# Kernel optimization log

Hardware: AMD Instinct MI355X
Metric: run time of the kernel (lower is better)

## Reference

```python
import jax, jax.numpy as jnp
import numpy as np

B, N, E, K = 8, 4096, 1, 3
F = [16, 32, 16]
MLP_HID, MLP_OUT = 64, 1


def graph_filter(x, S, h, b):
    # x: [B, Fin, N], S: [E, N, N], h: [Fout, E, K, Fin], b: [Fout, 1]
    Bx, Fin, Nx = x.shape
    Ex, Kx = h.shape[1], h.shape[2]
    cur = jnp.broadcast_to(x[:, None], (Bx, Ex, Fin, Nx))  # tap 0: z = x
    zs = [cur]
    for _ in range(Kx - 1):
        cur = jnp.einsum('enm,befm->befn', S, cur)  # diffuse one hop
        zs.append(cur)
    z = jnp.stack(zs, axis=2)  # [B, E, K, Fin, N]
    return jnp.einsum('gekf,bekfn->bgn', h, z) + b[None]  # [B, Fout, N]


def gnn_layer(x, S, h, b, n_out):
    # GraphFilter -> ReLU -> NoPool (select first n_out nodes)
    return jax.nn.relu(graph_filter(x, S, h, b))[:, :, :n_out]


def setup_inputs() -> dict:
    key = jax.random.key(0)
    ks = jax.random.split(key, 16)
    sN = np.float32(1.0 / np.sqrt(N))
    x = jax.random.normal(ks[0], (B, F[0], N), dtype=jnp.float32)
    S_clique = jax.random.normal(ks[1], (E, N, N), dtype=jnp.float32) * sN
    S_line = jax.random.normal(ks[2], (E, N, N), dtype=jnp.float32) * sN

    def w(k, fo, fi):
        s = np.float32(1.0 / np.sqrt(fi * K))
        return jax.random.normal(k, (fo, E, K, fi), dtype=jnp.float32) * s

    Wc1, bc1 = w(ks[3], F[1], F[0]), jnp.zeros((F[1], 1), jnp.float32)
    Wc2, bc2 = w(ks[4], F[2], F[1]), jnp.zeros((F[2], 1), jnp.float32)
    Wl1, bl1 = w(ks[5], F[1], F[0]), jnp.zeros((F[1], 1), jnp.float32)
    Wl2, bl2 = w(ks[6], F[2], F[1]), jnp.zeros((F[2], 1), jnp.float32)
    d_in = N * F[-1]
    Wm1 = jax.random.normal(ks[7], (MLP_HID, d_in), dtype=jnp.float32) * np.float32(1.0 / np.sqrt(d_in))
    bm1 = jnp.zeros((MLP_HID,), jnp.float32)
    Wm2 = jax.random.normal(ks[8], (MLP_OUT, MLP_HID), dtype=jnp.float32) * np.float32(1.0 / np.sqrt(MLP_HID))
    bm2 = jnp.zeros((MLP_OUT,), jnp.float32)
    return {'x': x, 'S_clique': S_clique, 'S_line': S_line,
            'Wc1': Wc1, 'bc1': bc1, 'Wc2': Wc2, 'bc2': bc2,
            'Wl1': Wl1, 'bl1': bl1, 'Wl2': Wl2, 'bl2': bl2,
            'Wm1': Wm1, 'bm1': bm1, 'Wm2': Wm2, 'bm2': bm2}


def reference(x, S_clique, S_line, Wc1, bc1, Wc2, bc2, Wl1, bl1, Wl2, bl2, Wm1, bm1, Wm2, bm2):
    # clique-expansion branch (L=2 layers)
    y = gnn_layer(x, S_clique, Wc1, bc1, N)
    y = gnn_layer(y, S_clique, Wc2, bc2, N)
    # line-expansion branch (L=2 layers)
    y = gnn_layer(y, S_line, Wl1, bl1, N)
    y = gnn_layer(y, S_line, Wl2, bl2, N)
    yFlat = y.reshape(y.shape[0], -1)  # [B, F[-1]*N] (row-major matches torch)
    h = jax.nn.relu(yFlat @ Wm1.T + bm1)
    return h @ Wm2.T + bm2  # [B, 1]
```

## Files before the change

kernel.cpp:

```cpp
#include <hip/hip_runtime.h>


#define NN 4096
#define BB 8

typedef unsigned short u16;
typedef unsigned int   u32;

typedef __attribute__((ext_vector_type(8))) short bf16x8;
typedef __attribute__((ext_vector_type(4))) float f32x4;

__device__ __forceinline__ u16 f2bf(float f) {
    union { float f; u32 i; } c; c.f = f;
    u32 i = c.i;
    u32 r = (i + 0x7FFFu + ((i >> 16) & 1u)) >> 16;
    return (u16)r;
}
__device__ __forceinline__ float bf2f(u16 u) {
    union { u32 i; float f; } c; c.i = ((u32)u) << 16; return c.f;
}
__device__ __forceinline__ u32 pack2bf(float lo, float hi) {
    return (u32)f2bf(lo) | ((u32)f2bf(hi) << 16);
}

__device__ __forceinline__ void gload_lds16(const u16* g, u16* l) {
    __builtin_amdgcn_global_load_lds(
        (__attribute__((address_space(1))) void*)g,
        (__attribute__((address_space(3))) void*)l, 16, 0, 0);
}

__global__ __launch_bounds__(256) void cvt_x(const float* __restrict__ in,
                                             u16* __restrict__ out)
{
    const int i = (blockIdx.x * 256 + threadIdx.x) * 8;
    float4 a = *(const float4*)(in + i);
    float4 b = *(const float4*)(in + i + 4);
    uint4 o;
    o.x = pack2bf(a.x, a.y); o.y = pack2bf(a.z, a.w);
    o.z = pack2bf(b.x, b.y); o.w = pack2bf(b.z, b.w);
    *(uint4*)(out + i) = o;
}

template <int ITERS>
__global__ __launch_bounds__(256) void diffuse_cvtB(const u16* __restrict__ Z,
                                                    const float* __restrict__ Sf,
                                                    u16* __restrict__ Part,
                                                    u16* __restrict__ Sb)
{
    __shared__ u16 As[2 * 128 * 64];
    __shared__ u16 Bs[2 * 64 * 64];

    const int bx    = blockIdx.x;
    const int ntile = ((bx & 7) << 3) | (bx >> 3);
    const int nBase = ntile * 64;
    const int mBase = blockIdx.y * 128;
    const int tid   = threadIdx.x;
    const int lane  = tid & 63;
    const int wv    = tid >> 6;
    const int quad  = lane >> 4;
    const int l16   = lane & 15;

    const int kStart = (int)blockIdx.z * (ITERS * 64);

    const int rl   = lane >> 3;
    const int gsl  = lane & 7;
    const int gsrc = gsl ^ rl;

    f32x4 acc[2][4];
#pragma unroll
    for (int i = 0; i < 2; ++i)
#pragma unroll
        for (int j = 0; j < 4; ++j) acc[i][j] = (f32x4){0.f, 0.f, 0.f, 0.f};

    auto stageA = [&](int buf, int k0) {
#pragma unroll
        for (int j = 0; j < 4; ++j) {
            const int rb = (wv * 4 + j) * 8;
            gload_lds16(Z + (size_t)(mBase + rb + rl) * NN + k0 + gsrc * 8,
                        &As[buf * 8192 + rb * 64]);
        }
    };

    float4 fB[2][2];
    auto loadB = [&](int k0) {
#pragma unroll
        for (int j = 0; j < 2; ++j) {
            const int row = nBase + (wv * 2 + j) * 8 + rl;
            const float* p = Sf + (size_t)row * NN + k0 + gsrc * 8;
            fB[j][0] = *(const float4*)p;
            fB[j][1] = *(const float4*)(p + 4);
        }
    };
    auto writeB = [&](int buf, int k0) {
#pragma unroll
        for (int j = 0; j < 2; ++j) {
            const int rloc = (wv * 2 + j) * 8 + rl;
            bf16x8 v;
            v[0] = (short)f2bf(fB[j][0].x); v[1] = (short)f2bf(fB[j][0].y);
            v[2] = (short)f2bf(fB[j][0].z); v[3] = (short)f2bf(fB[j][0].w);
            v[4] = (short)f2bf(fB[j][1].x); v[5] = (short)f2bf(fB[j][1].y);
            v[6] = (short)f2bf(fB[j][1].z); v[7] = (short)f2bf(fB[j][1].w);
            *(bf16x8*)&Bs[buf * 4096 + rloc * 64 + gsl * 8] = v;
            *(bf16x8*)&Sb[(size_t)(nBase + rloc) * NN + k0 + gsrc * 8] = v;
        }
    };

    auto compute = [&](int buf) {
#pragma unroll
        for (int s = 0; s < 2; ++s) {
            const int g = s * 4 + quad;
            bf16x8 af[2], bf[4];
#pragma unroll
            for (int mi = 0; mi < 2; ++mi) {
                const int r = wv * 32 + mi * 16 + l16;
                af[mi] = *(const bf16x8*)&As[buf * 8192 + r * 64 + ((g ^ (r & 7)) << 3)];
            }
#pragma unroll
            for (int ni = 0; ni < 4; ++ni) {
                const int r = ni * 16 + l16;
                bf[ni] = *(const bf16x8*)&Bs[buf * 4096 + r * 64 + ((g ^ (r & 7)) << 3)];
            }
#pragma unroll
            for (int mi = 0; mi < 2; ++mi)
#pragma unroll
                for (int ni = 0; ni < 4; ++ni)
                    acc[mi][ni] = __builtin_amdgcn_mfma_f32_16x16x32_bf16(
                        af[mi], bf[ni], acc[mi][ni], 0, 0, 0);
        }
    };

    loadB(kStart);
    stageA(0, kStart);
    writeB(0, kStart);
    __syncthreads();

#pragma unroll
    for (int i = 0; i < ITERS; ++i) {
        const int cur = i & 1;
        if (i + 1 < ITERS) {
            stageA(cur ^ 1, kStart + (i + 1) * 64);
            loadB(kStart + (i + 1) * 64);
        }
        compute(cur);
        if (i + 1 < ITERS) writeB(cur ^ 1, kStart + (i + 1) * 64);
        __syncthreads();
    }

    u16* tb = &As[wv * 2304];
#pragma unroll
    for (int mi = 0; mi < 2; ++mi)
#pragma unroll
        for (int ni = 0; ni < 4; ++ni)
#pragma unroll
            for (int i = 0; i < 4; ++i)
                tb[(mi * 16 + quad * 4 + i) * 72 + ni * 16 + l16] =
                    f2bf(acc[mi][ni][i]);

    const size_t plane = (size_t)gridDim.y * 128 * NN;
    u16* pp = Part + (size_t)blockIdx.z * plane;
    const int row0g = mBase + wv * 32;
#pragma unroll
    for (int j = 0; j < 4; ++j) {
        const int r = (lane >> 3) + j * 8;
        const int c = (lane & 7) * 8;
        bf16x8 v = *(const bf16x8*)&tb[r * 72 + c];
        *(bf16x8*)&pp[(size_t)(row0g + r) * NN + nBase + c] = v;
    }
}

template <int ITERS>
__global__ __launch_bounds__(256) void diffuse(const u16* __restrict__ Z,
                                               const u16* __restrict__ S,
                                               u16* __restrict__ Part)
{
    __shared__ u16 As[3 * 128 * 64];
    __shared__ u16 Bs[3 * 64 * 64];

    const int bx    = blockIdx.x;
    const int ntile = ((bx & 7) << 3) | (bx >> 3);
    const int nBase = ntile * 64;
    const int mBase = blockIdx.y * 128;
    const int tid   = threadIdx.x;
    const int lane  = tid & 63;
    const int wv    = tid >> 6;
    const int quad  = lane >> 4;
    const int l16   = lane & 15;

    const int kStart = (int)blockIdx.z * (ITERS * 64);

    const int rl   = lane >> 3;
    const int gsl  = lane & 7;
    const int gsrc = gsl ^ rl;

    f32x4 acc[2][4];
#pragma unroll
    for (int i = 0; i < 2; ++i)
#pragma unroll
        for (int j = 0; j < 4; ++j) acc[i][j] = (f32x4){0.f, 0.f, 0.f, 0.f};

    auto stage = [&](int buf, int k0) {
#pragma unroll
        for (int j = 0; j < 4; ++j) {
            const int rb = (wv * 4 + j) * 8;
            gload_lds16(Z + (size_t)(mBase + rb + rl) * NN + k0 + gsrc * 8,
                        &As[buf * 8192 + rb * 64]);
        }
#pragma unroll
        for (int j = 0; j < 2; ++j) {
            const int rb = (wv * 2 + j) * 8;
            gload_lds16(S + (size_t)(nBase + rb + rl) * NN + k0 + gsrc * 8,
                        &Bs[buf * 4096 + rb * 64]);
        }
    };

    auto compute = [&](int buf) {
#pragma unroll
        for (int s = 0; s < 2; ++s) {
            const int g = s * 4 + quad;
            bf16x8 af[2], bf[4];
#pragma unroll
            for (int mi = 0; mi < 2; ++mi) {
                const int r = wv * 32 + mi * 16 + l16;
                af[mi] = *(const bf16x8*)&As[buf * 8192 + r * 64 + ((g ^ (r & 7)) << 3)];
            }
#pragma unroll
            for (int ni = 0; ni < 4; ++ni) {
                const int r = ni * 16 + l16;
                bf[ni] = *(const bf16x8*)&Bs[buf * 4096 + r * 64 + ((g ^ (r & 7)) << 3)];
            }
#pragma unroll
            for (int mi = 0; mi < 2; ++mi)
#pragma unroll
                for (int ni = 0; ni < 4; ++ni)
                    acc[mi][ni] = __builtin_amdgcn_mfma_f32_16x16x32_bf16(
                        af[mi], bf[ni], acc[mi][ni], 0, 0, 0);
        }
    };

    stage(0, kStart);
    stage(1, kStart + 64);

#pragma unroll
    for (int i = 0; i < ITERS; ++i) {
        if (i + 2 < ITERS) stage((i + 2) % 3, kStart + (i + 2) * 64);
        if (i < ITERS - 2)
            asm volatile("s_waitcnt vmcnt(12)" ::: "memory");
        else if (i == ITERS - 2)
            asm volatile("s_waitcnt vmcnt(6)" ::: "memory");
        else
            asm volatile("s_waitcnt vmcnt(0)" ::: "memory");
        __builtin_amdgcn_s_barrier();
        compute(i % 3);
        if (i + 1 < ITERS) __builtin_amdgcn_s_barrier();
    }

    asm volatile("s_waitcnt lgkmcnt(0)" ::: "memory");
    __builtin_amdgcn_s_barrier();

    u16* tb = &As[wv * 2304];
#pragma unroll
    for (int mi = 0; mi < 2; ++mi)
#pragma unroll
        for (int ni = 0; ni < 4; ++ni)
#pragma unroll
            for (int i = 0; i < 4; ++i)
                tb[(mi * 16 + quad * 4 + i) * 72 + ni * 16 + l16] =
                    f2bf(acc[mi][ni][i]);

    const size_t plane = (size_t)gridDim.y * 128 * NN;
    u16* pp = Part + (size_t)blockIdx.z * plane;
    const int row0g = mBase + wv * 32;
#pragma unroll
    for (int j = 0; j < 4; ++j) {
        const int r = (lane >> 3) + j * 8;
        const int c = (lane & 7) * 8;
        bf16x8 v = *(const bf16x8*)&tb[r * 72 + c];
        *(bf16x8*)&pp[(size_t)(row0g + r) * NN + nBase + c] = v;
    }
}

template <int KS>
__global__ __launch_bounds__(256) void reduce_part(const u16* __restrict__ part,
                                                   int planeElems,
                                                   u16* __restrict__ outb)
{
    const int base   = (blockIdx.x * 256 + threadIdx.x) * 8;
    const int stride = gridDim.x * 256 * 8;
    for (int i = base; i < planeElems; i += stride) {
        float s[8];
#pragma unroll
        for (int e = 0; e < 8; ++e) s[e] = 0.f;
#pragma unroll
        for (int p = 0; p < KS; ++p) {
            uint4 v = *(const uint4*)(part + (size_t)p * planeElems + i);
            const u32 w[4] = {v.x, v.y, v.z, v.w};
#pragma unroll
            for (int q = 0; q < 4; ++q) {
                union { u32 i; float f; } lo, hi;
                lo.i = w[q] << 16;
                hi.i = w[q] & 0xFFFF0000u;
                s[q * 2]     += lo.f;
                s[q * 2 + 1] += hi.f;
            }
        }
        uint4 o;
        o.x = (u32)f2bf(s[0]) | ((u32)f2bf(s[1]) << 16);
        o.y = (u32)f2bf(s[2]) | ((u32)f2bf(s[3]) << 16);
        o.z = (u32)f2bf(s[4]) | ((u32)f2bf(s[5]) << 16);
        o.w = (u32)f2bf(s[6]) | ((u32)f2bf(s[7]) << 16);
        *(uint4*)(outb + i) = o;
    }
}

template <int FIN, int FOUT, int KS>
__global__ __launch_bounds__(256) void combine_relu(
    const u16* __restrict__ z0, const u16* __restrict__ z1,
    const u16* __restrict__ part2, int planeElems,
    const float* __restrict__ W, const float* __restrict__ bias,
    u16* __restrict__ out)
{
    __shared__ float hs[FOUT * 3 * FIN];
    __shared__ float bs[FOUT];
    for (int i = threadIdx.x; i < FOUT * 3 * FIN; i += 256) hs[i] = W[i];
    if (threadIdx.x < FOUT) bs[threadIdx.x] = bias[threadIdx.x];
    __syncthreads();

    const int nb = NN / 256;
    const int b  = blockIdx.x / nb;
    const int n  = (blockIdx.x % nb) * 256 + threadIdx.x;

    float zv[3][FIN];
    const u16* zp0 = z0 + (size_t)b * FIN * NN + n;
    const u16* zp1 = z1 + (size_t)b * FIN * NN + n;
    const u16* zp2 = part2 + (size_t)b * FIN * NN + n;
#pragma unroll
    for (int f = 0; f < FIN; ++f) {
        zv[0][f] = bf2f(zp0[(size_t)f * NN]);
        zv[1][f] = bf2f(zp1[(size_t)f * NN]);
        float s = 0.f;
#pragma unroll
        for (int p = 0; p < KS; ++p)
            s += bf2f(zp2[(size_t)p * planeElems + (size_t)f * NN]);
        zv[2][f] = s;
    }

    u16* op = out + (size_t)b * FOUT * NN + n;
    for (int g = 0; g < FOUT; ++g) {
        float acc = bs[g];
#pragma unroll
        for (int k = 0; k < 3; ++k)
#pragma unroll
            for (int f = 0; f < FIN; ++f)
                acc = fmaf(hs[(g * 3 + k) * FIN + f], zv[k][f], acc);
        op[(size_t)g * NN] = f2bf(fmaxf(acc, 0.f));
    }
}

__global__ __launch_bounds__(256) void mlp1(const u16* __restrict__ y,
                                            const float* __restrict__ Wm1,
                                            float* __restrict__ h1p)
{
    const int j    = blockIdx.x;
    const int base = blockIdx.y * 8192;
    const int D    = 16 * NN;

    float acc[BB];
#pragma unroll
    for (int b = 0; b < BB; ++b) acc[b] = 0.f;

    const float* wrow = Wm1 + (size_t)j * D + base;
    for (int idx = threadIdx.x * 8; idx < 8192; idx += 256 * 8) {
        float4 w0 = *(const float4*)(wrow + idx);
        float4 w1 = *(const float4*)(wrow + idx + 4);
#pragma unroll
        for (int b = 0; b < BB; ++b) {
            uint4 yv = *(const uint4*)(y + (size_t)b * D + base + idx);
            union { u32 i; float f; } c[8];
            c[0].i = yv.x << 16; c[1].i = yv.x & 0xFFFF0000u;
            c[2].i = yv.y << 16; c[3].i = yv.y & 0xFFFF0000u;
            c[4].i = yv.z << 16; c[5].i = yv.z & 0xFFFF0000u;
            c[6].i = yv.w << 16; c[7].i = yv.w & 0xFFFF0000u;
            acc[b] = fmaf(w0.x, c[0].f, acc[b]);
            acc[b] = fmaf(w0.y, c[1].f, acc[b]);
            acc[b] = fmaf(w0.z, c[2].f, acc[b]);
            acc[b] = fmaf(w0.w, c[3].f, acc[b]);
            acc[b] = fmaf(w1.x, c[4].f, acc[b]);
            acc[b] = fmaf(w1.y, c[5].f, acc[b]);
            acc[b] = fmaf(w1.z, c[6].f, acc[b]);
            acc[b] = fmaf(w1.w, c[7].f, acc[b]);
        }
    }

    __shared__ float red[BB][4];
    const int lane = threadIdx.x & 63;
    const int w    = threadIdx.x >> 6;
#pragma unroll
    for (int b = 0; b < BB; ++b) {
        float v = acc[b];
        for (int off = 32; off > 0; off >>= 1) v += __shfl_down(v, off, 64);
        if (lane == 0) red[b][w] = v;
    }
    __syncthreads();
    if (threadIdx.x < BB) {
        const int b = threadIdx.x;
        h1p[blockIdx.y * (BB * 64) + b * 64 + j] =
            red[b][0] + red[b][1] + red[b][2] + red[b][3];
    }
}

__global__ void mlp2(const float* __restrict__ h1p,
                     const float* __restrict__ bm1,
                     const float* __restrict__ Wm2,
                     const float* __restrict__ bm2, float* __restrict__ out)
{
    const int lane = threadIdx.x;
    const float w    = Wm2[lane];
    const float b1   = bm1[lane];
    const float bias = bm2[0];
    for (int b = 0; b < BB; ++b) {
        float h = 0.f;
#pragma unroll
        for (int p = 0; p < 8; ++p) h += h1p[p * (BB * 64) + b * 64 + lane];
        float v = fmaxf(h + b1, 0.f) * w;
        for (int off = 32; off > 0; off >>= 1) v += __shfl_down(v, off, 64);
        if (lane == 0) out[b] = v + bias;
    }
}

extern "C" void kernel_launch(void* const* d_in, const int* in_sizes, int n_in,
                              void* d_out, int out_size, void* d_ws, size_t ws_size,
                              hipStream_t stream)
{
    const float* x   = (const float*)d_in[0];
    const float* Sc  = (const float*)d_in[1];
    const float* Sl  = (const float*)d_in[2];
    const float* Wc1 = (const float*)d_in[3];
    const float* bc1 = (const float*)d_in[4];
    const float* Wc2 = (const float*)d_in[5];
    const float* bc2 = (const float*)d_in[6];
    const float* Wl1 = (const float*)d_in[7];
    const float* bl1 = (const float*)d_in[8];
    const float* Wl2 = (const float*)d_in[9];
    const float* bl2 = (const float*)d_in[10];
    const float* Wm1 = (const float*)d_in[11];
    const float* bm1 = (const float*)d_in[12];
    const float* Wm2 = (const float*)d_in[13];
    const float* bm2 = (const float*)d_in[14];
    float* out = (float*)d_out;

    char* ws = (char*)d_ws;
    u16*   part = (u16*)(ws);
    u16*   zb1  = (u16*)(ws + (8u  << 20));
    u16*   yPa  = (u16*)(ws + (12u << 20));
    u16*   yPb  = (u16*)(ws + (14u << 20));
    float* h1p  = (float*)(ws + (16u << 20));
    u16*   Scb  = (u16*)(ws + (17u << 20));
    u16*   Slb  = Scb + (size_t)NN * NN;

    const dim3 blk(256);
    const dim3 gridCmb(BB * NN / 256);
    const dim3 g2(64, 1, 8);
    const dim3 g4(64, 2, 4);
    const int  pl128 = 128 * NN;
    const int  pl256 = 256 * NN;

    cvt_x<<<256, blk, 0, stream>>>(x, yPa);

    diffuse_cvtB<8><<<g2, blk, 0, stream>>>(yPa, Sc, part, Scb);
    reduce_part<8><<<256, blk, 0, stream>>>(part, pl128, zb1);
    diffuse<8><<<g2, blk, 0, stream>>>(zb1, Scb, part);
    combine_relu<16, 32, 8><<<gridCmb, blk, 0, stream>>>(yPa, zb1, part, pl128,
                                                         Wc1, bc1, yPb);
    diffuse<16><<<g4, blk, 0, stream>>>(yPb, Scb, part);
    reduce_part<4><<<512, blk, 0, stream>>>(part, pl256, zb1);
    diffuse<16><<<g4, blk, 0, stream>>>(zb1, Scb, part);
    combine_relu<32, 16, 4><<<gridCmb, blk, 0, stream>>>(yPb, zb1, part, pl256,
                                                         Wc2, bc2, yPa);
    diffuse_cvtB<8><<<g2, blk, 0, stream>>>(yPa, Sl, part, Slb);
    reduce_part<8><<<256, blk, 0, stream>>>(part, pl128, zb1);
    diffuse<8><<<g2, blk, 0, stream>>>(zb1, Slb, part);
    combine_relu<16, 32, 8><<<gridCmb, blk, 0, stream>>>(yPa, zb1, part, pl128,
                                                         Wl1, bl1, yPb);
    diffuse<16><<<g4, blk, 0, stream>>>(yPb, Slb, part);
    reduce_part<4><<<512, blk, 0, stream>>>(part, pl256, zb1);
    diffuse<16><<<g4, blk, 0, stream>>>(zb1, Slb, part);
    combine_relu<32, 16, 4><<<gridCmb, blk, 0, stream>>>(yPb, zb1, part, pl256,
                                                         Wl2, bl2, yPa);
    mlp1<<<dim3(64, 8), blk, 0, stream>>>(yPa, Wm1, h1p);
    mlp2<<<1, 64, 0, stream>>>(h1p, bm1, Wm2, bm2, out);
}
```

Measured before the change: 368.4 us.

## Enlarge diffusion GEMM tiles to 128x128 with deeper split-K

Both diffusion GEMM kernels move from a 128x64 output tile to a 128x128 tile, with each wave computing a 64x64 sub-tile (4x4 MFMA accumulators). This halves the number of times Z is re-read across N tiles. The split-K factor is doubled to keep the grid large, so there are more partial planes to reduce and the workspace layout changes. The plain diffuse kernel drops its triple-buffered pipeline with fine-grained vmcnt waits for a simpler double buffer with a full wait each iteration, which risks exposing load latency. The bf16 copy of S is now shared by both branches.

```diff
diff --git a/kernel.cpp b/kernel.cpp
--- a/kernel.cpp
+++ b/kernel.cpp
@@ -42,23 +42,23 @@
 }
 
 template <int ITERS>
-__global__ __launch_bounds__(256) void diffuse_cvtB(const u16* __restrict__ Z,
-                                                    const float* __restrict__ Sf,
-                                                    u16* __restrict__ Part,
-                                                    u16* __restrict__ Sb)
-{
-    __shared__ u16 As[2 * 128 * 64];
-    __shared__ u16 Bs[2 * 64 * 64];
+__global__ __launch_bounds__(256) void diffuse(const u16* __restrict__ Z,
+                                               const u16* __restrict__ S,
+                                               u16* __restrict__ Part)
+{
+    __shared__ u16 L[4 * 128 * 64];
 
     const int bx    = blockIdx.x;
-    const int ntile = ((bx & 7) << 3) | (bx >> 3);
-    const int nBase = ntile * 64;
+    const int ntile = ((bx & 7) << 2) | (bx >> 3);
+    const int nBase = ntile * 128;
     const int mBase = blockIdx.y * 128;
     const int tid   = threadIdx.x;
     const int lane  = tid & 63;
     const int wv    = tid >> 6;
     const int quad  = lane >> 4;
     const int l16   = lane & 15;
+    const int wr    = (wv >> 1) * 64;
+    const int wc    = (wv & 1) * 64;
 
     const int kStart = (int)blockIdx.z * (ITERS * 64);
 
@@ -66,42 +66,20 @@
     const int gsl  = lane & 7;
     const int gsrc = gsl ^ rl;
 
-    f32x4 acc[2][4];
-#pragma unroll
-    for (int i = 0; i < 2; ++i)
+    f32x4 acc[4][4];
+#pragma unroll
+    for (int i = 0; i < 4; ++i)
 #pragma unroll
         for (int j = 0; j < 4; ++j) acc[i][j] = (f32x4){0.f, 0.f, 0.f, 0.f};
 
-    auto stageA = [&](int buf, int k0) {
+    auto stage = [&](int buf, int k0) {
 #pragma unroll
         for (int j = 0; j < 4; ++j) {
-            const int rb = (wv * 4 + j) * 8;
+            const int rb = wv * 32 + j * 8;
             gload_lds16(Z + (size_t)(mBase + rb + rl) * NN + k0 + gsrc * 8,
-                        &As[buf * 8192 + rb * 64]);
-        }
-    };
-
-    float4 fB[2][2];
-    auto loadB = [&](int k0) {
-#pragma unroll
-        for (int j = 0; j < 2; ++j) {
-            const int row = nBase + (wv * 2 + j) * 8 + rl;
-            const float* p = Sf + (size_t)row * NN + k0 + gsrc * 8;
-            fB[j][0] = *(const float4*)p;
-            fB[j][1] = *(const float4*)(p + 4);
-        }
-    };
-    auto writeB = [&](int buf, int k0) {
-#pragma unroll
-        for (int j = 0; j < 2; ++j) {
-            const int rloc = (wv * 2 + j) * 8 + rl;
-            bf16x8 v;
-            v[0] = (short)f2bf(fB[j][0].x); v[1] = (short)f2bf(fB[j][0].y);
-            v[2] = (short)f2bf(fB[j][0].z); v[3] = (short)f2bf(fB[j][0].w);
-            v[4] = (short)f2bf(fB[j][1].x); v[5] = (short)f2bf(fB[j][1].y);
-            v[6] = (short)f2bf(fB[j][1].z); v[7] = (short)f2bf(fB[j][1].w);
-            *(bf16x8*)&Bs[buf * 4096 + rloc * 64 + gsl * 8] = v;
-            *(bf16x8*)&Sb[(size_t)(nBase + rloc) * NN + k0 + gsrc * 8] = v;
+                        &L[buf * 8192 + rb * 64]);
+            gload_lds16(S + (size_t)(nBase + rb + rl) * NN + k0 + gsrc * 8,
+                        &L[16384 + buf * 8192 + rb * 64]);
         }
     };
 
@@ -109,19 +87,19 @@
 #pragma unroll
         for (int s = 0; s < 2; ++s) {
             const int g = s * 4 + quad;
-            bf16x8 af[2], bf[4];
-#pragma unroll
-            for (int mi = 0; mi < 2; ++mi) {
-                const int r = wv * 32 + mi * 16 + l16;
-                af[mi] = *(const bf16x8*)&As[buf * 8192 + r * 64 + ((g ^ (r & 7)) << 3)];
+            bf16x8 af[4], bf[4];
+#pragma unroll
+            for (int mi = 0; mi < 4; ++mi) {
+                const int r = wr + mi * 16 + l16;
+                af[mi] = *(const bf16x8*)&L[buf * 8192 + r * 64 + ((g ^ (r & 7)) << 3)];
             }
 #pragma unroll
             for (int ni = 0; ni < 4; ++ni) {
-                const int r = ni * 16 + l16;
-                bf[ni] = *(const bf16x8*)&Bs[buf * 4096 + r * 64 + ((g ^ (r & 7)) << 3)];
+                const int r = wc + ni * 16 + l16;
+                bf[ni] = *(const bf16x8*)&L[16384 + buf * 8192 + r * 64 + ((g ^ (r & 7)) << 3)];
             }
 #pragma unroll
-            for (int mi = 0; mi < 2; ++mi)
+            for (int mi = 0; mi < 4; ++mi)
 #pragma unroll
                 for (int ni = 0; ni < 4; ++ni)
                     acc[mi][ni] = __builtin_amdgcn_mfma_f32_16x16x32_bf16(
@@ -129,26 +107,21 @@
         }
     };
 
-    loadB(kStart);
-    stageA(0, kStart);
-    writeB(0, kStart);
-    __syncthreads();
-
+    stage(0, kStart);
 #pragma unroll
     for (int i = 0; i < ITERS; ++i) {
-        const int cur = i & 1;
-        if (i + 1 < ITERS) {
-            stageA(cur ^ 1, kStart + (i + 1) * 64);
-            loadB(kStart + (i + 1) * 64);
-        }
-        compute(cur);
-        if (i + 1 < ITERS) writeB(cur ^ 1, kStart + (i + 1) * 64);
-        __syncthreads();
-    }
-
-    u16* tb = &As[wv * 2304];
-#pragma unroll
-    for (int mi = 0; mi < 2; ++mi)
+        asm volatile("s_waitcnt vmcnt(0)" ::: "memory");
+        __builtin_amdgcn_s_barrier();
+        if (i + 1 < ITERS) stage((i + 1) & 1, kStart + (i + 1) * 64);
+        compute(i & 1);
+    }
+
+    asm volatile("s_waitcnt lgkmcnt(0)" ::: "memory");
+    __builtin_amdgcn_s_barrier();
+
+    u16* tb = &L[wv * 4608];
+#pragma unroll
+    for (int mi = 0; mi < 4; ++mi)
 #pragma unroll
         for (int ni = 0; ni < 4; ++ni)
 #pragma unroll
@@ -158,33 +131,36 @@
 
     const size_t plane = (size_t)gridDim.y * 128 * NN;
     u16* pp = Part + (size_t)blockIdx.z * plane;
-    const int row0g = mBase + wv * 32;
-#pragma unroll
-    for (int j = 0; j < 4; ++j) {
+    const int row0g = mBase + wr;
+    const int col0g = nBase + wc;
+#pragma unroll
+    for (int j = 0; j < 8; ++j) {
         const int r = (lane >> 3) + j * 8;
         const int c = (lane & 7) * 8;
         bf16x8 v = *(const bf16x8*)&tb[r * 72 + c];
-        *(bf16x8*)&pp[(size_t)(row0g + r) * NN + nBase + c] = v;
+        *(bf16x8*)&pp[(size_t)(row0g + r) * NN + col0g + c] = v;
     }
 }
 
 template <int ITERS>
-__global__ __launch_bounds__(256) void diffuse(const u16* __restrict__ Z,
-                                               const u16* __restrict__ S,
-                                               u16* __restrict__ Part)
-{
-    __shared__ u16 As[3 * 128 * 64];
-    __shared__ u16 Bs[3 * 64 * 64];
+__global__ __launch_bounds__(256) void diffuse_cvtB(const u16* __restrict__ Z,
+                                                    const float* __restrict__ Sf,
+                                                    u16* __restrict__ Part,
+                                                    u16* __restrict__ Sb)
+{
+    __shared__ u16 L[4 * 128 * 64];
 
     const int bx    = blockIdx.x;
-    const int ntile = ((bx & 7) << 3) | (bx >> 3);
-    const int nBase = ntile * 64;
+    const int ntile = ((bx & 7) << 2) | (bx >> 3);
+    const int nBase = ntile * 128;
     const int mBase = blockIdx.y * 128;
     const int tid   = threadIdx.x;
     const int lane  = tid & 63;
     const int wv    = tid >> 6;
     const int quad  = lane >> 4;
     const int l16   = lane & 15;
+    const int wr    = (wv >> 1) * 64;
+    const int wc    = (wv & 1) * 64;
 
     const int kStart = (int)blockIdx.z * (ITERS * 64);
 
@@ -192,24 +168,42 @@
     const int gsl  = lane & 7;
     const int gsrc = gsl ^ rl;
 
-    f32x4 acc[2][4];
-#pragma unroll
-    for (int i = 0; i < 2; ++i)
+    f32x4 acc[4][4];
+#pragma unroll
+    for (int i = 0; i < 4; ++i)
 #pragma unroll
         for (int j = 0; j < 4; ++j) acc[i][j] = (f32x4){0.f, 0.f, 0.f, 0.f};
 
-    auto stage = [&](int buf, int k0) {
+    auto stageA = [&](int buf, int k0) {
 #pragma unroll
         for (int j = 0; j < 4; ++j) {
-            const int rb = (wv * 4 + j) * 8;
+            const int rb = wv * 32 + j * 8;
             gload_lds16(Z + (size_t)(mBase + rb + rl) * NN + k0 + gsrc * 8,
-                        &As[buf * 8192 + rb * 64]);
-        }
-#pragma unroll
-        for (int j = 0; j < 2; ++j) {
-            const int rb = (wv * 2 + j) * 8;
-            gload_lds16(S + (size_t)(nBase + rb + rl) * NN + k0 + gsrc * 8,
-                        &Bs[buf * 4096 + rb * 64]);
+                        &L[buf * 8192 + rb * 64]);
+        }
+    };
+
+    float4 fB[4][2];
+    auto loadB = [&](int k0) {
+#pragma unroll
+        for (int j = 0; j < 4; ++j) {
+            const int row = nBase + wv * 32 + j * 8 + rl;
+            const float* p = Sf + (size_t)row * NN + k0 + gsrc * 8;
+            fB[j][0] = *(const float4*)p;
+            fB[j][1] = *(const float4*)(p + 4);
+        }
+    };
+    auto writeB = [&](int buf, int k0) {
+#pragma unroll
+        for (int j = 0; j < 4; ++j) {
+            const int rloc = wv * 32 + j * 8 + rl;
+            bf16x8 v;
+            v[0] = (short)f2bf(fB[j][0].x); v[1] = (short)f2bf(fB[j][0].y);
+            v[2] = (short)f2bf(fB[j][0].z); v[3] = (short)f2bf(fB[j][0].w);
+            v[4] = (short)f2bf(fB[j][1].x); v[5] = (short)f2bf(fB[j][1].y);
+            v[6] = (short)f2bf(fB[j][1].z); v[7] = (short)f2bf(fB[j][1].w);
+            *(bf16x8*)&L[16384 + buf * 8192 + rloc * 64 + gsl * 8] = v;
+            *(bf16x8*)&Sb[(size_t)(nBase + rloc) * NN + k0 + gsrc * 8] = v;
         }
     };
 
@@ -217,19 +211,19 @@
 #pragma unroll
         for (int s = 0; s < 2; ++s) {
             const int g = s * 4 + quad;
-            bf16x8 af[2], bf[4];
-#pragma unroll
-            for (int mi = 0; mi < 2; ++mi) {
-                const int r = wv * 32 + mi * 16 + l16;
-                af[mi] = *(const bf16x8*)&As[buf * 8192 + r * 64 + ((g ^ (r & 7)) << 3)];
+            bf16x8 af[4], bf[4];
+#pragma unroll
+            for (int mi = 0; mi < 4; ++mi) {
+                const int r = wr + mi * 16 + l16;
+                af[mi] = *(const bf16x8*)&L[buf * 8192 + r * 64 + ((g ^ (r & 7)) << 3)];
             }
 #pragma unroll
             for (int ni = 0; ni < 4; ++ni) {
-                const int r = ni * 16 + l16;
-                bf[ni] = *(const bf16x8*)&Bs[buf * 4096 + r * 64 + ((g ^ (r & 7)) << 3)];
+                const int r = wc + ni * 16 + l16;
+                bf[ni] = *(const bf16x8*)&L[16384 + buf * 8192 + r * 64 + ((g ^ (r & 7)) << 3)];
             }
 #pragma unroll
-            for (int mi = 0; mi < 2; ++mi)
+            for (int mi = 0; mi < 4; ++mi)
 #pragma unroll
                 for (int ni = 0; ni < 4; ++ni)
                     acc[mi][ni] = __builtin_amdgcn_mfma_f32_16x16x32_bf16(
@@ -237,29 +231,23 @@
         }
     };
 
-    stage(0, kStart);
-    stage(1, kStart + 64);
+    loadB(kStart);
+    stageA(0, kStart);
+    writeB(0, kStart);
+    __syncthreads();
 
 #pragma unroll
     for (int i = 0; i < ITERS; ++i) {
-        if (i + 2 < ITERS) stage((i + 2) % 3, kStart + (i + 2) * 64);
-        if (i < ITERS - 2)
-            asm volatile("s_waitcnt vmcnt(12)" ::: "memory");
-        else if (i == ITERS - 2)
-            asm volatile("s_waitcnt vmcnt(6)" ::: "memory");
-        else
-            asm volatile("s_waitcnt vmcnt(0)" ::: "memory");
-        __builtin_amdgcn_s_barrier();
-        compute(i % 3);
-        if (i + 1 < ITERS) __builtin_amdgcn_s_barrier();
-    }
-
-    asm volatile("s_waitcnt lgkmcnt(0)" ::: "memory");
-    __builtin_amdgcn_s_barrier();
-
-    u16* tb = &As[wv * 2304];
-#pragma unroll
-    for (int mi = 0; mi < 2; ++mi)
+        const int k1 = kStart + (i + 1) * 64;
+        if (i + 1 < ITERS) { stageA((i + 1) & 1, k1); loadB(k1); }
+        compute(i & 1);
+        if (i + 1 < ITERS) writeB((i + 1) & 1, k1);
+        __syncthreads();
+    }
+
+    u16* tb = &L[wv * 4608];
+#pragma unroll
+    for (int mi = 0; mi < 4; ++mi)
 #pragma unroll
         for (int ni = 0; ni < 4; ++ni)
 #pragma unroll
@@ -269,13 +257,14 @@
 
     const size_t plane = (size_t)gridDim.y * 128 * NN;
     u16* pp = Part + (size_t)blockIdx.z * plane;
-    const int row0g = mBase + wv * 32;
-#pragma unroll
-    for (int j = 0; j < 4; ++j) {
+    const int row0g = mBase + wr;
+    const int col0g = nBase + wc;
+#pragma unroll
+    for (int j = 0; j < 8; ++j) {
         const int r = (lane >> 3) + j * 8;
         const int c = (lane & 7) * 8;
         bf16x8 v = *(const bf16x8*)&tb[r * 72 + c];
-        *(bf16x8*)&pp[(size_t)(row0g + r) * NN + nBase + c] = v;
+        *(bf16x8*)&pp[(size_t)(row0g + r) * NN + col0g + c] = v;
     }
 }
 
@@ -450,41 +439,40 @@
 
     char* ws = (char*)d_ws;
     u16*   part = (u16*)(ws);
-    u16*   zb1  = (u16*)(ws + (8u  << 20));
-    u16*   yPa  = (u16*)(ws + (12u << 20));
-    u16*   yPb  = (u16*)(ws + (14u << 20));
-    float* h1p  = (float*)(ws + (16u << 20));
-    u16*   Scb  = (u16*)(ws + (17u << 20));
-    u16*   Slb  = Scb + (size_t)NN * NN;
+    u16*   zb1  = (u16*)(ws + (16u << 20));
+    u16*   yPa  = (u16*)(ws + (18u << 20));
+    u16*   yPb  = (u16*)(ws + (20u << 20));
+    float* h1p  = (float*)(ws + (22u << 20));
+    u16*   Sb   = (u16*)(ws + (23u << 20));
 
     const dim3 blk(256);
     const dim3 gridCmb(BB * NN / 256);
-    const dim3 g2(64, 1, 8);
-    const dim3 g4(64, 2, 4);
+    const dim3 g128(32, 1, 16);
+    const dim3 g256(32, 2, 8);
     const int  pl128 = 128 * NN;
     const int  pl256 = 256 * NN;
 
     cvt_x<<<256, blk, 0, stream>>>(x, yPa);
 
-    diffuse_cvtB<8><<<g2, blk, 0, stream>>>(yPa, Sc, part, Scb);
-    reduce_part<8><<<256, blk, 0, stream>>>(part, pl128, zb1);
-    diffuse<8><<<g2, blk, 0, stream>>>(zb1, Scb, part);
-    combine_relu<16, 32, 8><<<gridCmb, blk, 0, stream>>>(yPa, zb1, part, pl128,
-                                                         Wc1, bc1, yPb);
-    diffuse<16><<<g4, blk, 0, stream>>>(yPb, Scb, part);
-    reduce_part<4><<<512, blk, 0, stream>>>(part, pl256, zb1);
-    diffuse<16><<<g4, blk, 0, stream>>>(zb1, Scb, part);
-    combine_relu<32, 16, 4><<<gridCmb, blk, 0, stream>>>(yPb, zb1, part, pl256,
+    diffuse_cvtB<4><<<g128, blk, 0, stream>>>(yPa, Sc, part, Sb);
+    reduce_part<16><<<256, blk, 0, stream>>>(part, pl128, zb1);
+    diffuse<4><<<g128, blk, 0, stream>>>(zb1, Sb, part);
+    combine_relu<16, 32, 16><<<gridCmb, blk, 0, stream>>>(yPa, zb1, part, pl128,
+                                                          Wc1, bc1, yPb);
+    diffuse<8><<<g256, blk, 0, stream>>>(yPb, Sb, part);
+    reduce_part<8><<<512, blk, 0, stream>>>(part, pl256, zb1);
+    diffuse<8><<<g256, blk, 0, stream>>>(zb1, Sb, part);
+    combine_relu<32, 16, 8><<<gridCmb, blk, 0, stream>>>(yPb, zb1, part, pl256,
                                                          Wc2, bc2, yPa);
-    diffuse_cvtB<8><<<g2, blk, 0, stream>>>(yPa, Sl, part, Slb);
-    reduce_part<8><<<256, blk, 0, stream>>>(part, pl128, zb1);
-    diffuse<8><<<g2, blk, 0, stream>>>(zb1, Slb, part);
-    combine_relu<16, 32, 8><<<gridCmb, blk, 0, stream>>>(yPa, zb1, part, pl128,
-                                                         Wl1, bl1, yPb);
-    diffuse<16><<<g4, blk, 0, stream>>>(yPb, Slb, part);
-    reduce_part<4><<<512, blk, 0, stream>>>(part, pl256, zb1);
-    diffuse<16><<<g4, blk, 0, stream>>>(zb1, Slb, part);
-    combine_relu<32, 16, 4><<<gridCmb, blk, 0, stream>>>(yPb, zb1, part, pl256,
+    diffuse_cvtB<4><<<g128, blk, 0, stream>>>(yPa, Sl, part, Sb);
+    reduce_part<16><<<256, blk, 0, stream>>>(part, pl128, zb1);
+    diffuse<4><<<g128, blk, 0, stream>>>(zb1, Sb, part);
+    combine_relu<16, 32, 16><<<gridCmb, blk, 0, stream>>>(yPa, zb1, part, pl128,
+                                                          Wl1, bl1, yPb);
+    diffuse<8><<<g256, blk, 0, stream>>>(yPb, Sb, part);
+    reduce_part<8><<<512, blk, 0, stream>>>(part, pl256, zb1);
+    diffuse<8><<<g256, blk, 0, stream>>>(zb1, Sb, part);
+    combine_relu<32, 16, 8><<<gridCmb, blk, 0, stream>>>(yPb, zb1, part, pl256,
                                                          Wl2, bl2, yPa);
     mlp1<<<dim3(64, 8), blk, 0, stream>>>(yPa, Wm1, h1p);
     mlp2<<<1, 64, 0, stream>>>(h1p, bm1, Wm2, bm2, out);
```

Result: slower. 400.8 us (+8.8%).
